# Optimization experiments

Hardware: AMD Instinct MI355X
Metric: run time of the kernel (lower is better)

## Reference

```python
import jax, jax.numpy as jnp
import numpy as np

B, DIN, DOUT = 16, 64, 64
P1_, P2_, P3_ = 64, 32, 16
BN_EPS = 1e-5


def setup_inputs() -> dict:
    key = jax.random.key(0)
    ks = jax.random.split(key, 8)
    A = jax.random.normal(ks[0], (B, DIN, P1_, P2_, P3_), dtype=jnp.float32)
    ini_p = float(np.sqrt(3.0 / DOUT / DIN))
    ini_qk = float(np.sqrt(1.0 / DOUT / DIN))
    def uni(k, s):
        return jax.random.uniform(k, (DOUT, DIN), dtype=jnp.float32, minval=-s, maxval=s)
    return {
        "A": A,
        "P1": uni(ks[1], ini_p),
        "P2": uni(ks[2], ini_p),
        "P3": uni(ks[3], ini_p),
        "P4": uni(ks[4], ini_p),
        "q": uni(ks[5], ini_qk),
        "k": uni(ks[6], ini_qk),
        "gamma": jnp.ones((DOUT,), jnp.float32),
        "beta": jnp.zeros((DOUT,), jnp.float32),
        "permutation_size1": P1_,
        "permutation_size2": P2_,
        "permutation_size3": P3_,
        "BATCH_SIZE": B,
    }


def reference(A, P1, P2, P3, P4, q, k, gamma, beta,
              permutation_size1, permutation_size2, permutation_size3, BATCH_SIZE):
    b = BATCH_SIZE
    dout = P1.shape[0]
    p1, p2, p3 = permutation_size1, permutation_size2, permutation_size3
    # branch 1: full per-element channel mix  [B, dout, p1, p2, p3]
    A1 = jnp.einsum('oi,bixyz->boxyz', P1, A)
    # branch 2: mean over p3, project, broadcast over p3
    A2 = jnp.einsum('oi,bixy->boxy', P2, A.mean(-1))[..., None]
    # branch 3: mean over p2, project, broadcast over p2
    A3 = jnp.einsum('oi,bixz->boxz', P3, A.mean(-2))[:, :, :, None, :]
    # attention over p1 with flattened (p2*p3) as the contraction axis
    Q = jnp.einsum('oi,bixyz->boxyz', q, A).reshape(b, dout, p1, p2 * p3)
    K = jnp.einsum('oi,bixyz->boxyz', k, A).reshape(b, dout, p1, p2 * p3)
    Alpha = jnp.einsum('bcxm,bcym->bcxy', Q, K)  # [B, dout, p1, p1]
    Alpha_norm = jnp.abs(Alpha) / jnp.linalg.norm(Alpha, axis=3, keepdims=True)
    V = jnp.einsum('oi,bixyz->boxyz', P4, A).reshape(b, dout, p1, p2 * p3)
    Y = jnp.einsum('bcxy,bcym->bcxm', Alpha_norm, V).reshape(b, dout, p1, p2, p3)
    out = A1 + 0.1 * A2 + 0.1 * A3 + 0.1 * Y
    out = jax.nn.relu(out)
    # BatchNorm3d (training-mode batch statistics, biased variance)
    mean = out.mean(axis=(0, 2, 3, 4), keepdims=True)
    var = out.var(axis=(0, 2, 3, 4), keepdims=True)
    out = (out - mean) * jax.lax.rsqrt(var + BN_EPS)
    out = out * gamma[None, :, None, None, None] + beta[None, :, None, None, None]
    return out
```

## Files before the change

### kernel.cpp

```cpp
#include <hip/hip_runtime.h>

typedef __attribute__((ext_vector_type(8))) short short8;
typedef __attribute__((ext_vector_type(4))) float f32x4;
typedef __attribute__((ext_vector_type(8))) unsigned short u16x8;
typedef __attribute__((ext_vector_type(4))) unsigned short u16x4;
typedef __attribute__((ext_vector_type(4))) unsigned int u32x4;
typedef unsigned short u16;

#define DEVINL __device__ __forceinline__

DEVINL u16 f2bf(float f) {
  unsigned u = __builtin_bit_cast(unsigned, f);
  unsigned r = (u + 0x7fffu + ((u >> 16) & 1u)) >> 16;
  return (u16)r;
}
DEVINL float bf2f(u16 h) {
  unsigned u = ((unsigned)h) << 16;
  return __builtin_bit_cast(float, u);
}
DEVINL unsigned pk2(float a, float b) {
  return (unsigned)f2bf(a) | ((unsigned)f2bf(b) << 16);
}
DEVINL int swzc(int row, int chunk) { return chunk ^ ((row ^ (row >> 3)) & 7); }
DEVINL int tile_byte(int row, int chunk) { return row * 128 + swzc(row, chunk) * 16; }

__global__ void kw_convert(const float* __restrict__ P1, const float* __restrict__ q,
                           const float* __restrict__ k, const float* __restrict__ P4,
                           const float* __restrict__ P2, const float* __restrict__ P3,
                           u16* __restrict__ Wbf) {
  int t = threadIdx.x;
  const float* srcs[6] = {P1, q, k, P4, P2, P3};
  for (int w = 0; w < 6; ++w)
    for (int e = t; e < 4096; e += 256) Wbf[w * 4096 + e] = f2bf(srcs[w][e]);
}

__global__ __launch_bounds__(512) void k_projA(
    const float* __restrict__ A, const u16* __restrict__ Wbf, u16* __restrict__ A1,
    u16* __restrict__ Q, u16* __restrict__ Km, u16* __restrict__ V,
    float* __restrict__ A2g, float* __restrict__ m2p, int g0) {
  __shared__ __align__(16) u16 tile[256 * 64];
  __shared__ __align__(16) u16 meanT[16 * 64];
  const int t = threadIdx.x;
  const int w = t >> 6, l = t & 63;
  const int lr = l & 15, lh = l >> 4;
  const int T = blockIdx.x, bg = blockIdx.y;
  const int x = T >> 1, h = T & 1;
  const long bglob = g0 + bg;

  const int m = w & 3, sh = w >> 2;
  const u16* wb = Wbf + m * 4096;
  short8 wf[4][2];
#pragma unroll
  for (int ot = 0; ot < 4; ++ot)
#pragma unroll
    for (int ks = 0; ks < 2; ++ks)
      wf[ot][ks] = *(const short8*)(wb + (ot * 16 + lr) * 64 + ks * 32 + lh * 8);
  u16* outp = (m == 0) ? A1 : (m == 1) ? Q : (m == 2) ? Km : V;
  outp += (long)bg * 64 * 32768;
  const int odd = lh & 1;
  const int p8 = (lh >> 1) * 8;

  {
    const int s4 = t & 31, i4 = t >> 5;
    const float* ap =
        A + (bglob * 64 + i4 * 4) * 32768 + (long)x * 512 + h * 256 + s4 * 4;
#pragma unroll
    for (int si = 0; si < 2; ++si) {
      f32x4 v0 = *(const f32x4*)(ap + si * 128);
      f32x4 v1 = *(const f32x4*)(ap + si * 128 + 32768);
      f32x4 v2 = *(const f32x4*)(ap + si * 128 + 65536);
      f32x4 v3 = *(const f32x4*)(ap + si * 128 + 98304);
#pragma unroll
      for (int e = 0; e < 4; ++e) {
        int s = si * 128 + s4 * 4 + e;
        u16x4 pk = {f2bf(v0[e]), f2bf(v1[e]), f2bf(v2[e]), f2bf(v3[e])};
        *(u16x4*)((char*)tile + tile_byte(s, i4 >> 1) + (i4 & 1) * 8) = pk;
      }
    }
  }
  __syncthreads();

  {
    const int ic = t & 7, zq = (t >> 3) & 3, y16 = t >> 5;
    float acc[8] = {0, 0, 0, 0, 0, 0, 0, 0};
#pragma unroll
    for (int zz = 0; zz < 4; ++zz) {
      int row = y16 * 16 + zq * 4 + zz;
      u16x8 v = *(const u16x8*)((const char*)tile + tile_byte(row, ic));
#pragma unroll
      for (int e = 0; e < 8; ++e) acc[e] += bf2f(v[e]);
    }
#pragma unroll
    for (int e = 0; e < 8; ++e) {
      acc[e] += __shfl_xor(acc[e], 8);
      acc[e] += __shfl_xor(acc[e], 16);
    }
    if (zq == 0) {
      u16x8 pk;
#pragma unroll
      for (int e = 0; e < 8; ++e) pk[e] = f2bf(acc[e] * (1.0f / 16.0f));
      *(u16x8*)((char*)meanT + tile_byte(y16, ic)) = pk;
    }
  }
  {
    const int ic = t & 7, yg = (t >> 3) & 3, z = t >> 5;
    float acc[8] = {0, 0, 0, 0, 0, 0, 0, 0};
#pragma unroll
    for (int yy = 0; yy < 4; ++yy) {
      int row = (yg * 4 + yy) * 16 + z;
      u16x8 v = *(const u16x8*)((const char*)tile + tile_byte(row, ic));
#pragma unroll
      for (int e = 0; e < 8; ++e) acc[e] += bf2f(v[e]);
    }
#pragma unroll
    for (int e = 0; e < 8; ++e) {
      acc[e] += __shfl_xor(acc[e], 8);
      acc[e] += __shfl_xor(acc[e], 16);
    }
    if (yg == 0) {
      float* mp = m2p + (((long)bg * 64 + x) * 2 + h) * 1024 + z * 64 + ic * 8;
      *(f32x4*)(mp) = (f32x4){acc[0], acc[1], acc[2], acc[3]};
      *(f32x4*)(mp + 4) = (f32x4){acc[4], acc[5], acc[6], acc[7]};
    }
  }
  __syncthreads();

  if (w == 0) {
    const u16* wb2 = Wbf + 4 * 4096;
    f32x4 acc2[4];
#pragma unroll
    for (int ot = 0; ot < 4; ++ot) acc2[ot] = {0.0f, 0.0f, 0.0f, 0.0f};
#pragma unroll
    for (int ks = 0; ks < 2; ++ks) {
      short8 mf = *(const short8*)((const char*)meanT + tile_byte(lr, ks * 4 + lh));
#pragma unroll
      for (int ot = 0; ot < 4; ++ot) {
        short8 w2f = *(const short8*)(wb2 + (ot * 16 + lr) * 64 + ks * 32 + lh * 8);
        acc2[ot] = __builtin_amdgcn_mfma_f32_16x16x32_bf16(w2f, mf, acc2[ot], 0, 0, 0);
      }
    }
#pragma unroll
    for (int ot = 0; ot < 4; ++ot)
#pragma unroll
      for (int r = 0; r < 4; ++r) {
        int o = ot * 16 + lh * 4 + r;
        A2g[(((long)bg * 64 + o) * 64 + x) * 32 + h * 16 + lr] = acc2[ot][r];
      }
  }

  for (int stp = 0; stp < 4; ++stp) {
    const int srowE = sh * 128 + stp * 32 + lr;
    const int srowO = srowE + 16;
    short8 aE0 = *(const short8*)((const char*)tile + tile_byte(srowE, lh));
    short8 aE1 = *(const short8*)((const char*)tile + tile_byte(srowE, 4 + lh));
    short8 aO0 = *(const short8*)((const char*)tile + tile_byte(srowO, lh));
    short8 aO1 = *(const short8*)((const char*)tile + tile_byte(srowO, 4 + lh));
    const int sbase = x * 512 + h * 256 + sh * 128 + stp * 32 + odd * 16 + p8;
#pragma unroll
    for (int ot = 0; ot < 4; ++ot) {
      f32x4 accE = {0.0f, 0.0f, 0.0f, 0.0f}, accO = {0.0f, 0.0f, 0.0f, 0.0f};
      accE = __builtin_amdgcn_mfma_f32_16x16x32_bf16(aE0, wf[ot][0], accE, 0, 0, 0);
      accE = __builtin_amdgcn_mfma_f32_16x16x32_bf16(aE1, wf[ot][1], accE, 0, 0, 0);
      accO = __builtin_amdgcn_mfma_f32_16x16x32_bf16(aO0, wf[ot][0], accO, 0, 0, 0);
      accO = __builtin_amdgcn_mfma_f32_16x16x32_bf16(aO1, wf[ot][1], accO, 0, 0, 0);
      unsigned pE0 = pk2(accE[0], accE[1]), pE1 = pk2(accE[2], accE[3]);
      unsigned pO0 = pk2(accO[0], accO[1]), pO1 = pk2(accO[2], accO[3]);
      unsigned rE0 = __shfl_xor((int)pE0, 16), rE1 = __shfl_xor((int)pE1, 16);
      unsigned rO0 = __shfl_xor((int)pO0, 16), rO1 = __shfl_xor((int)pO1, 16);
      u32x4 sv;
      if (odd) sv = (u32x4){rO0, rO1, pO0, pO1};
      else     sv = (u32x4){pE0, pE1, rE0, rE1};
      *(u32x4*)(outp + (long)(ot * 16 + lr) * 32768 + sbase) = sv;
    }
  }
}

__global__ __launch_bounds__(256) void k_a3fin(const float* __restrict__ m2p,
                                               const float* __restrict__ P3,
                                               float* __restrict__ A3g, int g0) {
  __shared__ float m2s[16 * 65];
  const int t = threadIdx.x;
  const int x = blockIdx.x, bg = blockIdx.y;
  const float* mp = m2p + ((long)bg * 64 + x) * 2048;
  {
    int e = t * 4;
    int z = e >> 6, i = e & 63;
    f32x4 v0 = *(const f32x4*)(mp + e);
    f32x4 v1 = *(const f32x4*)(mp + 1024 + e);
#pragma unroll
    for (int j = 0; j < 4; ++j) m2s[z * 65 + i + j] = (v0[j] + v1[j]) * (1.0f / 32.0f);
  }
  __syncthreads();
  const int z = t & 15, og = t >> 4;
#pragma unroll
  for (int oo = 0; oo < 4; ++oo) {
    int o = og * 4 + oo;
    float acc = 0.0f;
#pragma unroll 8
    for (int i = 0; i < 64; ++i) acc += P3[o * 64 + i] * m2s[z * 65 + i];
    A3g[(((long)bg * 64 + o) * 64 + x) * 16 + z] = acc;
  }
}

__global__ __launch_bounds__(256) void k_attn(const u16* __restrict__ Qg,
                                              const u16* __restrict__ Kg,
                                              const u16* __restrict__ Vg,
                                              const u16* __restrict__ A1g,
                                              const float* __restrict__ A2g,
                                              const float* __restrict__ A3g,
                                              u16* __restrict__ outbf,
                                              float* __restrict__ partials, int g0) {
  __shared__ __align__(16) u16 Qc[4096], Kc[4096], Vt[4096], An[4096];
  __shared__ float red[8];
  const int t = threadIdx.x, w = t >> 6, l = t & 63;
  const int lr = l & 15, lh = l >> 4;
  const int c = blockIdx.x, bg = blockIdx.y;
  const long bglob = g0 + bg;
  const long base = ((long)bg * 64 + c) * 32768;
  const u16* Qp = Qg + base;
  const u16* Kp = Kg + base;
  const u16* Vp = Vg + base;
  const u16* A1p = A1g + base;

  f32x4 accA[4];
#pragma unroll
  for (int yt = 0; yt < 4; ++yt) accA[yt] = {0.0f, 0.0f, 0.0f, 0.0f};

  const int srow = t >> 3, scc = t & 7;
  for (int mc = 0; mc < 8; ++mc) {
#pragma unroll
    for (int it = 0; it < 2; ++it) {
      int row = srow + it * 32;
      int gch = scc ^ ((row ^ (row >> 3)) & 7);
      u16x8 qv = *(const u16x8*)(Qp + row * 512 + mc * 64 + gch * 8);
      u16x8 kv = *(const u16x8*)(Kp + row * 512 + mc * 64 + gch * 8);
      *(u16x8*)((char*)Qc + row * 128 + scc * 16) = qv;
      *(u16x8*)((char*)Kc + row * 128 + scc * 16) = kv;
    }
    __syncthreads();
    short8 qf[2];
#pragma unroll
    for (int ks = 0; ks < 2; ++ks)
      qf[ks] = *(const short8*)((const char*)Qc + tile_byte(16 * w + lr, ks * 4 + lh));
#pragma unroll
    for (int ks = 0; ks < 2; ++ks)
#pragma unroll
      for (int yt = 0; yt < 4; ++yt) {
        short8 kf = *(const short8*)((const char*)Kc + tile_byte(yt * 16 + lr, ks * 4 + lh));
        accA[yt] = __builtin_amdgcn_mfma_f32_16x16x32_bf16(qf[ks], kf, accA[yt], 0, 0, 0);
      }
    __syncthreads();
  }

  float rsq[4];
#pragma unroll
  for (int r = 0; r < 4; ++r) {
    float s = 0.0f;
#pragma unroll
    for (int yt = 0; yt < 4; ++yt) s += accA[yt][r] * accA[yt][r];
#pragma unroll
    for (int msk = 1; msk < 16; msk <<= 1) s += __shfl_xor(s, msk);
    rsq[r] = rsqrtf(s);
  }
#pragma unroll
  for (int yt = 0; yt < 4; ++yt)
#pragma unroll
    for (int r = 0; r < 4; ++r) {
      int xr = 16 * w + 4 * lh + r;
      int y = yt * 16 + lr;
      *(u16*)((char*)An + xr * 128 + swzc(xr, y >> 3) * 16 + (y & 7) * 2) =
          f2bf(fabsf(accA[yt][r]) * rsq[r]);
    }

  float ls = 0.0f, lsq = 0.0f;
  const float* A2p = A2g + ((long)bg * 64 + c) * 2048;
  const float* A3p = A3g + ((long)bg * 64 + c) * 1024;
  u16* outp = outbf + (bglob * 64 + c) * 32768;
  const int m4 = t & 15, y4 = t >> 4;
  const int x = 16 * w + lr;

  for (int mc = 0; mc < 8; ++mc) {
    __syncthreads();
    u16x4 vr[4];
#pragma unroll
    for (int r = 0; r < 4; ++r)
      vr[r] = *(const u16x4*)(Vp + (y4 * 4 + r) * 512 + mc * 64 + m4 * 4);
#pragma unroll
    for (int ci = 0; ci < 4; ++ci) {
      int mrow = m4 * 4 + ci;
      u16x4 pk = {vr[0][ci], vr[1][ci], vr[2][ci], vr[3][ci]};
      *(u16x4*)((char*)Vt + tile_byte(mrow, y4 >> 1) + (y4 & 1) * 8) = pk;
    }
    __syncthreads();

    f32x4 accY[4];
#pragma unroll
    for (int mt = 0; mt < 4; ++mt) accY[mt] = {0.0f, 0.0f, 0.0f, 0.0f};
#pragma unroll
    for (int ks = 0; ks < 2; ++ks) {
      short8 anf = *(const short8*)((const char*)An + tile_byte(16 * w + lr, ks * 4 + lh));
#pragma unroll
      for (int mt = 0; mt < 4; ++mt) {
        short8 vf = *(const short8*)((const char*)Vt + tile_byte(mt * 16 + lr, ks * 4 + lh));
        accY[mt] = __builtin_amdgcn_mfma_f32_16x16x32_bf16(vf, anf, accY[mt], 0, 0, 0);
      }
    }
    f32x4 a3v = *(const f32x4*)(A3p + x * 16 + lh * 4);
#pragma unroll
    for (int mt = 0; mt < 4; ++mt) {
      float a2v = A2p[x * 32 + mc * 4 + mt];
      int mbase = mc * 64 + mt * 16 + lh * 4;
      u16x4 a1v = *(const u16x4*)(A1p + x * 512 + mbase);
      u16x4 o;
#pragma unroll
      for (int r = 0; r < 4; ++r) {
        float val = bf2f(a1v[r]) + 0.1f * (a2v + a3v[r] + accY[mt][r]);
        val = fmaxf(val, 0.0f);
        o[r] = f2bf(val);
        ls += val;
        lsq += val * val;
      }
      *(u16x4*)(outp + x * 512 + mbase) = o;
    }
  }

#pragma unroll
  for (int off = 32; off > 0; off >>= 1) {
    ls += __shfl_xor(ls, off);
    lsq += __shfl_xor(lsq, off);
  }
  if (l == 0) {
    red[w] = ls;
    red[4 + w] = lsq;
  }
  __syncthreads();
  if (t == 0) {
    partials[2 * (bglob * 64 + c) + 0] = red[0] + red[1] + red[2] + red[3];
    partials[2 * (bglob * 64 + c) + 1] = red[4] + red[5] + red[6] + red[7];
  }
}

__global__ void k_stats(const float* __restrict__ partials, const float* __restrict__ gamma,
                        const float* __restrict__ beta, float* __restrict__ sb) {
  int c = threadIdx.x;
  if (c >= 64) return;
  float S = 0.0f, SQ = 0.0f;
  for (int b = 0; b < 16; ++b) {
    S += partials[2 * (b * 64 + c) + 0];
    SQ += partials[2 * (b * 64 + c) + 1];
  }
  const float N = 524288.0f;
  float mean = S / N;
  float var = SQ / N - mean * mean;
  float rs = rsqrtf(var + 1e-5f);
  float scale = gamma[c] * rs;
  sb[c] = scale;
  sb[64 + c] = beta[c] - mean * scale;
}

__global__ void k_bn(const u16* __restrict__ outbf, float* __restrict__ out,
                     const float* __restrict__ sb) {
  long idx = ((long)blockIdx.x * 256 + threadIdx.x) * 8;
  int c = (int)((idx >> 15) & 63);
  float scale = sb[c], bias = sb[64 + c];
  u16x8 v = *(const u16x8*)(outbf + idx);
  f32x4 o0, o1;
#pragma unroll
  for (int r = 0; r < 4; ++r) {
    o0[r] = bf2f(v[r]) * scale + bias;
    o1[r] = bf2f(v[4 + r]) * scale + bias;
  }
  *(f32x4*)(out + idx) = o0;
  *(f32x4*)(out + idx + 4) = o1;
}

extern "C" void kernel_launch(void* const* d_in, const int* in_sizes, int n_in, void* d_out,
                              int out_size, void* d_ws, size_t ws_size, hipStream_t stream) {
  (void)in_sizes; (void)n_in; (void)out_size;
  const float* A = (const float*)d_in[0];
  const float* P1 = (const float*)d_in[1];
  const float* P2 = (const float*)d_in[2];
  const float* P3 = (const float*)d_in[3];
  const float* P4 = (const float*)d_in[4];
  const float* q = (const float*)d_in[5];
  const float* k = (const float*)d_in[6];
  const float* gamma = (const float*)d_in[7];
  const float* beta = (const float*)d_in[8];
  float* out = (float*)d_out;
  char* ws = (char*)d_ws;

  u16* Wbf = (u16*)ws;
  float* partials = (float*)(ws + 49152);
  float* sb = (float*)(ws + 57344);
  const size_t GR = 65536;
  const size_t OUTBF = (size_t)16 * 64 * 32768 * 2;
  u16* outbf = (u16*)(ws + GR);
  const size_t SZ_M = (size_t)64 * 32768 * 2;
  const size_t SZ_A2 = (size_t)64 * 64 * 32 * 4;
  const size_t SZ_A3 = (size_t)64 * 64 * 16 * 4;
  const size_t SZ_M2 = (size_t)64 * 2 * 16 * 64 * 4;
  const size_t perb = 4 * SZ_M + SZ_A2 + SZ_A3 + SZ_M2;
  const size_t base0 = GR + OUTBF;
  int G = 1;
  if (ws_size > base0 + perb) G = (int)((ws_size - base0) / perb);
  if (G > 16) G = 16;
  if (G < 1) G = 1;

  u16* A1 = (u16*)(ws + base0);
  u16* Qw = (u16*)(ws + base0 + (size_t)G * SZ_M);
  u16* Kw = (u16*)(ws + base0 + (size_t)G * SZ_M * 2);
  u16* Vw = (u16*)(ws + base0 + (size_t)G * SZ_M * 3);
  float* A2 = (float*)(ws + base0 + (size_t)G * SZ_M * 4);
  float* A3 = (float*)((char*)A2 + (size_t)G * SZ_A2);
  float* m2p = (float*)((char*)A3 + (size_t)G * SZ_A3);

  kw_convert<<<1, 256, 0, stream>>>(P1, q, k, P4, P2, P3, Wbf);
  for (int g0 = 0; g0 < 16; g0 += G) {
    int Gc = (16 - g0) < G ? (16 - g0) : G;
    k_projA<<<dim3(128, Gc), 512, 0, stream>>>(A, Wbf, A1, Qw, Kw, Vw, A2, m2p, g0);
    k_a3fin<<<dim3(64, Gc), 256, 0, stream>>>(m2p, P3, A3, g0);
    k_attn<<<dim3(64, Gc), 256, 0, stream>>>(Qw, Kw, Vw, A1, A2, A3, outbf, partials, g0);
  }
  k_stats<<<1, 64, 0, stream>>>(partials, gamma, beta, sb);
  k_bn<<<16384, 256, 0, stream>>>(outbf, out, sb);
}
```

Baseline: 277.3 us.

## Load Q/K fragments directly from global and double-buffer V transpose

In the attention kernel the Q and K tiles are no longer staged through LDS. MFMA fragments are read straight from global memory, which removes two barriers per chunk and frees LDS. The V transpose now uses a double-buffered LDS tile with register prefetch of the next chunk, so one barrier per iteration is enough and the loads overlap the MFMA work. In the projection kernel the A2 mean-projection tail is moved after the main store loop, and the A3 load is hoisted out of the loop. Direct global loads of K fragments may be less coalesced and may repeat reads that L2 has to absorb.

New measurement: 288.0 us. 1.04x slower.

```diff
diff --git a/kernel.cpp b/kernel.cpp
--- a/kernel.cpp
+++ b/kernel.cpp
@@ -122,30 +122,6 @@
       *(f32x4*)(mp) = (f32x4){acc[0], acc[1], acc[2], acc[3]};
       *(f32x4*)(mp + 4) = (f32x4){acc[4], acc[5], acc[6], acc[7]};
     }
-  }
-  __syncthreads();
-
-  if (w == 0) {
-    const u16* wb2 = Wbf + 4 * 4096;
-    f32x4 acc2[4];
-#pragma unroll
-    for (int ot = 0; ot < 4; ++ot) acc2[ot] = {0.0f, 0.0f, 0.0f, 0.0f};
-#pragma unroll
-    for (int ks = 0; ks < 2; ++ks) {
-      short8 mf = *(const short8*)((const char*)meanT + tile_byte(lr, ks * 4 + lh));
-#pragma unroll
-      for (int ot = 0; ot < 4; ++ot) {
-        short8 w2f = *(const short8*)(wb2 + (ot * 16 + lr) * 64 + ks * 32 + lh * 8);
-        acc2[ot] = __builtin_amdgcn_mfma_f32_16x16x32_bf16(w2f, mf, acc2[ot], 0, 0, 0);
-      }
-    }
-#pragma unroll
-    for (int ot = 0; ot < 4; ++ot)
-#pragma unroll
-      for (int r = 0; r < 4; ++r) {
-        int o = ot * 16 + lh * 4 + r;
-        A2g[(((long)bg * 64 + o) * 64 + x) * 32 + h * 16 + lr] = acc2[ot][r];
-      }
   }
 
   for (int stp = 0; stp < 4; ++stp) {
@@ -173,6 +149,30 @@
       *(u32x4*)(outp + (long)(ot * 16 + lr) * 32768 + sbase) = sv;
     }
   }
+  __syncthreads();
+
+  if (w == 0) {
+    const u16* wb2 = Wbf + 4 * 4096;
+    f32x4 acc2[4];
+#pragma unroll
+    for (int ot = 0; ot < 4; ++ot) acc2[ot] = {0.0f, 0.0f, 0.0f, 0.0f};
+#pragma unroll
+    for (int ks = 0; ks < 2; ++ks) {
+      short8 mf = *(const short8*)((const char*)meanT + tile_byte(lr, ks * 4 + lh));
+#pragma unroll
+      for (int ot = 0; ot < 4; ++ot) {
+        short8 w2f = *(const short8*)(wb2 + (ot * 16 + lr) * 64 + ks * 32 + lh * 8);
+        acc2[ot] = __builtin_amdgcn_mfma_f32_16x16x32_bf16(w2f, mf, acc2[ot], 0, 0, 0);
+      }
+    }
+#pragma unroll
+    for (int ot = 0; ot < 4; ++ot)
+#pragma unroll
+      for (int r = 0; r < 4; ++r) {
+        int o = ot * 16 + lh * 4 + r;
+        A2g[(((long)bg * 64 + o) * 64 + x) * 32 + h * 16 + lr] = acc2[ot][r];
+      }
+  }
 }
 
 __global__ __launch_bounds__(256) void k_a3fin(const float* __restrict__ m2p,
@@ -210,7 +210,8 @@
                                               const float* __restrict__ A3g,
                                               u16* __restrict__ outbf,
                                               float* __restrict__ partials, int g0) {
-  __shared__ __align__(16) u16 Qc[4096], Kc[4096], Vt[4096], An[4096];
+  __shared__ __align__(16) u16 Vt[2][4096];
+  __shared__ __align__(16) u16 An[4096];
   __shared__ float red[8];
   const int t = threadIdx.x, w = t >> 6, l = t & 63;
   const int lr = l & 15, lh = l >> 4;
@@ -222,34 +223,31 @@
   const u16* Vp = Vg + base;
   const u16* A1p = A1g + base;
 
+  const int m4 = t & 15, y4 = t >> 4;
+
+  u16x4 vr[4];
+#pragma unroll
+  for (int r = 0; r < 4; ++r)
+    vr[r] = *(const u16x4*)(Vp + (y4 * 4 + r) * 512 + m4 * 4);
+
   f32x4 accA[4];
 #pragma unroll
   for (int yt = 0; yt < 4; ++yt) accA[yt] = {0.0f, 0.0f, 0.0f, 0.0f};
-
-  const int srow = t >> 3, scc = t & 7;
-  for (int mc = 0; mc < 8; ++mc) {
-#pragma unroll
-    for (int it = 0; it < 2; ++it) {
-      int row = srow + it * 32;
-      int gch = scc ^ ((row ^ (row >> 3)) & 7);
-      u16x8 qv = *(const u16x8*)(Qp + row * 512 + mc * 64 + gch * 8);
-      u16x8 kv = *(const u16x8*)(Kp + row * 512 + mc * 64 + gch * 8);
-      *(u16x8*)((char*)Qc + row * 128 + scc * 16) = qv;
-      *(u16x8*)((char*)Kc + row * 128 + scc * 16) = kv;
-    }
-    __syncthreads();
-    short8 qf[2];
-#pragma unroll
-    for (int ks = 0; ks < 2; ++ks)
-      qf[ks] = *(const short8*)((const char*)Qc + tile_byte(16 * w + lr, ks * 4 + lh));
-#pragma unroll
-    for (int ks = 0; ks < 2; ++ks)
+  {
+    const u16* Qrow = Qp + (16 * w + lr) * 512 + lh * 8;
+    const u16* Krow = Kp + lr * 512 + lh * 8;
+    for (int mc = 0; mc < 8; ++mc) {
+      const int cb = mc * 64;
+      short8 qf0 = *(const short8*)(Qrow + cb);
+      short8 qf1 = *(const short8*)(Qrow + cb + 32);
 #pragma unroll
       for (int yt = 0; yt < 4; ++yt) {
-        short8 kf = *(const short8*)((const char*)Kc + tile_byte(yt * 16 + lr, ks * 4 + lh));
-        accA[yt] = __builtin_amdgcn_mfma_f32_16x16x32_bf16(qf[ks], kf, accA[yt], 0, 0, 0);
-      }
-    __syncthreads();
+        short8 kf0 = *(const short8*)(Krow + yt * 16 * 512 + cb);
+        short8 kf1 = *(const short8*)(Krow + yt * 16 * 512 + cb + 32);
+        accA[yt] = __builtin_amdgcn_mfma_f32_16x16x32_bf16(qf0, kf0, accA[yt], 0, 0, 0);
+        accA[yt] = __builtin_amdgcn_mfma_f32_16x16x32_bf16(qf1, kf1, accA[yt], 0, 0, 0);
+      }
+    }
   }
 
   float rsq[4];
@@ -276,22 +274,26 @@
   const float* A2p = A2g + ((long)bg * 64 + c) * 2048;
   const float* A3p = A3g + ((long)bg * 64 + c) * 1024;
   u16* outp = outbf + (bglob * 64 + c) * 32768;
-  const int m4 = t & 15, y4 = t >> 4;
   const int x = 16 * w + lr;
+  const f32x4 a3v = *(const f32x4*)(A3p + x * 16 + lh * 4);
 
   for (int mc = 0; mc < 8; ++mc) {
-    __syncthreads();
-    u16x4 vr[4];
-#pragma unroll
-    for (int r = 0; r < 4; ++r)
-      vr[r] = *(const u16x4*)(Vp + (y4 * 4 + r) * 512 + mc * 64 + m4 * 4);
+    u16* vbuf = Vt[mc & 1];
 #pragma unroll
     for (int ci = 0; ci < 4; ++ci) {
       int mrow = m4 * 4 + ci;
       u16x4 pk = {vr[0][ci], vr[1][ci], vr[2][ci], vr[3][ci]};
-      *(u16x4*)((char*)Vt + tile_byte(mrow, y4 >> 1) + (y4 & 1) * 8) = pk;
-    }
-    __syncthreads();
+      *(u16x4*)((char*)vbuf + tile_byte(mrow, y4 >> 1) + (y4 & 1) * 8) = pk;
+    }
+    asm volatile("s_waitcnt lgkmcnt(0)" ::: "memory");
+    __builtin_amdgcn_s_barrier();
+    __builtin_amdgcn_sched_barrier(0);
+    if (mc < 7) {
+      const int nc = (mc + 1) * 64;
+#pragma unroll
+      for (int r = 0; r < 4; ++r)
+        vr[r] = *(const u16x4*)(Vp + (y4 * 4 + r) * 512 + nc + m4 * 4);
+    }
 
     f32x4 accY[4];
 #pragma unroll
@@ -301,11 +303,10 @@
       short8 anf = *(const short8*)((const char*)An + tile_byte(16 * w + lr, ks * 4 + lh));
 #pragma unroll
       for (int mt = 0; mt < 4; ++mt) {
-        short8 vf = *(const short8*)((const char*)Vt + tile_byte(mt * 16 + lr, ks * 4 + lh));
+        short8 vf = *(const short8*)((const char*)vbuf + tile_byte(mt * 16 + lr, ks * 4 + lh));
         accY[mt] = __builtin_amdgcn_mfma_f32_16x16x32_bf16(vf, anf, accY[mt], 0, 0, 0);
       }
     }
-    f32x4 a3v = *(const f32x4*)(A3p + x * 16 + lh * 4);
 #pragma unroll
     for (int mt = 0; mt < 4; ++mt) {
       float a2v = A2p[x * 32 + mc * 4 + mt];
```
